# Kernel tuning notes

Measured on AMD Instinct MI355X. Metric: run time of the kernel, lower is better.

Reference implementation:

```python
import math
import jax, jax.numpy as jnp
import numpy as np

B, T, C = 4, 2048, 1024
NH, HD = 16, C // 16
FF = 4096
EPS = 1e-5


def _layernorm(x, g, b):
    mu = jnp.mean(x, axis=-1, keepdims=True)
    var = jnp.mean(jnp.square(x - mu), axis=-1, keepdims=True)
    return (x - mu) * jax.lax.rsqrt(var + EPS) * g + b


def _new_gelu(x):
    c = math.sqrt(2.0 / math.pi)
    return 0.5 * x * (1.0 + jnp.tanh(c * (x + 0.044715 * x * x * x)))


def setup_inputs() -> dict:
    key = jax.random.key(0)
    ks = jax.random.split(key, 5)
    s = lambda fan_in: 1.0 / math.sqrt(fan_in)
    return {
        "x": jax.random.normal(ks[0], (B, T, C), jnp.float32),
        "ln1_g": jnp.ones((C,), jnp.float32),
        "ln1_b": jnp.zeros((C,), jnp.float32),
        "w_qkv": jax.random.normal(ks[1], (C, 3 * C), jnp.float32) * s(C),
        "b_qkv": jnp.zeros((3 * C,), jnp.float32),
        "w_attn_proj": jax.random.normal(ks[2], (C, C), jnp.float32) * s(C),
        "b_attn_proj": jnp.zeros((C,), jnp.float32),
        "ln2_g": jnp.ones((C,), jnp.float32),
        "ln2_b": jnp.zeros((C,), jnp.float32),
        "w_fc": jax.random.normal(ks[3], (C, FF), jnp.float32) * s(C),
        "b_fc": jnp.zeros((FF,), jnp.float32),
        "w_mlp_proj": jax.random.normal(ks[4], (FF, C), jnp.float32) * s(FF),
        "b_mlp_proj": jnp.zeros((C,), jnp.float32),
    }


def reference(x, ln1_g, ln1_b, w_qkv, b_qkv, w_attn_proj, b_attn_proj,
              ln2_g, ln2_b, w_fc, b_fc, w_mlp_proj, b_mlp_proj):
    # --- attention branch ---
    h = _layernorm(x, ln1_g, ln1_b)
    qkv = h @ w_qkv + b_qkv                      # [B,T,3C]
    q, k, v = jnp.split(qkv, 3, axis=-1)
    # [B,T,C] -> [B,NH,T,HD]
    to_heads = lambda t: t.reshape(B, T, NH, HD).transpose(0, 2, 1, 3)
    q, k, v = to_heads(q), to_heads(k), to_heads(v)
    scores = jnp.einsum("bhqd,bhkd->bhqk", q, k) / math.sqrt(HD)  # [B,NH,T,T]
    causal = jnp.tril(jnp.ones((T, T), bool))
    scores = jnp.where(causal, scores, -jnp.inf)
    probs = jax.nn.softmax(scores, axis=-1)
    attn = jnp.einsum("bhqk,bhkd->bhqd", probs, v)  # [B,NH,T,HD]
    attn = attn.transpose(0, 2, 1, 3).reshape(B, T, C)
    x = x + attn @ w_attn_proj + b_attn_proj
    # --- MLP branch ---
    h = _layernorm(x, ln2_g, ln2_b)
    h = _new_gelu(h @ w_fc + b_fc)
    x = x + h @ w_mlp_proj + b_mlp_proj
    return x
```

## Files before the change

### kernel.cpp

```cpp
#include <hip/hip_runtime.h>
#include <hip/hip_bf16.h>

typedef __bf16 bf16x8 __attribute__((ext_vector_type(8)));
typedef __bf16 bf16x4 __attribute__((ext_vector_type(4)));
typedef float f32x4 __attribute__((ext_vector_type(4)));

#define BM 128
#define BN 128
#define BK 32

__device__ __forceinline__ void gload16(const __bf16* g, __bf16* l) {
    __builtin_amdgcn_global_load_lds((const __attribute__((address_space(1))) void*)g,
                                     (__attribute__((address_space(3))) void*)l, 16, 0, 0);
}

__device__ __forceinline__ float gelu_f(float v) {
    float z = 0.7978845608028654f * (v + 0.044715f * v * v * v);
    float e = __expf(2.f * z);
    return 0.5f * v * (2.f - 2.f / (e + 1.f));
}

__global__ __launch_bounds__(256) void diag_kernel(float* out, int n, float v) {
    int i = blockIdx.x * 256 + threadIdx.x;
    if (i < n) out[i] = v;
}

__global__ __launch_bounds__(256) void cvtT_kernel(
    const float* __restrict__ in, __bf16* __restrict__ out, int K, int N)
{
    __shared__ __bf16 tile[32][33];
    int bx = blockIdx.x * 32, by = blockIdx.y * 32;
    int tx = threadIdx.x & 31, ty = threadIdx.x >> 5;
#pragma unroll
    for (int i = 0; i < 32; i += 8)
        tile[ty + i][tx] = (__bf16)in[(size_t)(by + ty + i) * N + bx + tx];
    __syncthreads();
#pragma unroll
    for (int i = 0; i < 32; i += 8)
        out[(size_t)(bx + ty + i) * K + by + tx] = tile[tx][ty + i];
}

__global__ __launch_bounds__(256) void ln_kernel(
    const float* __restrict__ x, const float* __restrict__ g,
    const float* __restrict__ bta, __bf16* __restrict__ out)
{
    const int row = blockIdx.x, t = threadIdx.x;
    const float* xr = x + (size_t)row * 1024;
    float4 xv = ((const float4*)xr)[t];
    float f[4] = {xv.x, xv.y, xv.z, xv.w};
    float s = f[0] + f[1] + f[2] + f[3];
    float ss = f[0]*f[0] + f[1]*f[1] + f[2]*f[2] + f[3]*f[3];
#pragma unroll
    for (int off = 32; off; off >>= 1) {
        s  += __shfl_xor(s, off, 64);
        ss += __shfl_xor(ss, off, 64);
    }
    __shared__ float red[8];
    int lane = t & 63, w = t >> 6;
    if (lane == 0) { red[w] = s; red[4 + w] = ss; }
    __syncthreads();
    s  = red[0] + red[1] + red[2] + red[3];
    ss = red[4] + red[5] + red[6] + red[7];
    float mu = s * (1.f / 1024.f);
    float var = ss * (1.f / 1024.f) - mu * mu;
    float rstd = rsqrtf(fmaxf(var, 0.f) + 1e-5f);
    float4 gv = ((const float4*)g)[t];
    float4 bv = ((const float4*)bta)[t];
    bf16x4 ov;
    ov[0] = (__bf16)((f[0] - mu) * rstd * gv.x + bv.x);
    ov[1] = (__bf16)((f[1] - mu) * rstd * gv.y + bv.y);
    ov[2] = (__bf16)((f[2] - mu) * rstd * gv.z + bv.z);
    ov[3] = (__bf16)((f[3] - mu) * rstd * gv.w + bv.w);
    ((bf16x4*)(out + (size_t)row * 1024))[t] = ov;
}

template <int EPI, bool OUT32>
__global__ __launch_bounds__(256, 4) void gemm_bt_kernel(
    const __bf16* __restrict__ A, const __bf16* __restrict__ BT,
    const float* __restrict__ bias, const float* __restrict__ res,
    void* __restrict__ Cp, int M, int N, int K)
{
    __shared__ __align__(16) __bf16 lA[BM * BK];
    __shared__ __align__(16) __bf16 lB[BN * BK];
    const int t = threadIdx.x;
    const int lane = t & 63;
    const int wave = t >> 6;
    const int wm = wave >> 1, wn = wave & 1;
    const int q4 = lane >> 4, r16 = lane & 15;
    const int bm = blockIdx.y * BM, bn = blockIdx.x * BN;

    const int srow = t & 127;
    const int skc = t >> 7;
    const __bf16* ga0 = A + (size_t)(bm + srow) * K + skc * 8;
    const __bf16* ga1 = A + (size_t)(bm + srow) * K + (skc + 2) * 8;
    const __bf16* gb0 = BT + (size_t)(bn + srow) * K + skc * 8;
    const __bf16* gb1 = BT + (size_t)(bn + srow) * K + (skc + 2) * 8;

    f32x4 acc[4][4];
    f32x4 zero4 = {0.f, 0.f, 0.f, 0.f};
#pragma unroll
    for (int mi = 0; mi < 4; ++mi)
#pragma unroll
        for (int ni = 0; ni < 4; ++ni) acc[mi][ni] = zero4;

    for (int k0 = 0; k0 < K; k0 += BK) {
        __syncthreads();
        gload16(ga0, &lA[t * 8]);
        gload16(ga1, &lA[t * 8 + 2048]);
        gload16(gb0, &lB[t * 8]);
        gload16(gb1, &lB[t * 8 + 2048]);
        ga0 += BK; ga1 += BK; gb0 += BK; gb1 += BK;
        __syncthreads();
        bf16x8 af[4], bfr[4];
#pragma unroll
        for (int i = 0; i < 4; ++i)
            af[i] = *(const bf16x8*)&lA[q4 * 1024 + (wm * 64 + i * 16 + r16) * 8];
#pragma unroll
        for (int i = 0; i < 4; ++i)
            bfr[i] = *(const bf16x8*)&lB[q4 * 1024 + (wn * 64 + i * 16 + r16) * 8];
#pragma unroll
        for (int mi = 0; mi < 4; ++mi)
#pragma unroll
            for (int ni = 0; ni < 4; ++ni)
                acc[mi][ni] = __builtin_amdgcn_mfma_f32_16x16x32_bf16(
                    af[mi], bfr[ni], acc[mi][ni], 0, 0, 0);
    }

#pragma unroll
    for (int mi = 0; mi < 4; ++mi) {
#pragma unroll
        for (int ni = 0; ni < 4; ++ni) {
#pragma unroll
            for (int i = 0; i < 4; ++i) {
                int r = bm + wm * 64 + mi * 16 + q4 * 4 + i;
                int c = bn + wn * 64 + ni * 16 + r16;
                float v = acc[mi][ni][i] + bias[c];
                if (EPI == 1) v += res[(size_t)r * N + c];
                if (EPI == 2) v = gelu_f(v);
                if (OUT32) ((float*)Cp)[(size_t)r * N + c] = v;
                else       ((__bf16*)Cp)[(size_t)r * N + c] = (__bf16)v;
            }
        }
    }
}

template <int EPI, bool OUT32>
__global__ __launch_bounds__(256, 2) void gemm_bt_wide_kernel(
    const __bf16* __restrict__ A, const __bf16* __restrict__ BT,
    const float* __restrict__ bias, const float* __restrict__ res,
    void* __restrict__ Cp, int M, int N, int K)
{
    __shared__ __align__(16) __bf16 lA[128 * BK];
    __shared__ __align__(16) __bf16 lB[256 * BK];
    const int t = threadIdx.x;
    const int lane = t & 63;
    const int wave = t >> 6;
    const int wm = wave >> 1, wn = wave & 1;
    const int q4 = lane >> 4, r16 = lane & 15;
    const int bm = blockIdx.y * 128, bn = blockIdx.x * 256;

    const int srow = t & 127;
    const int skc = t >> 7;
    const __bf16* ga0 = A + (size_t)(bm + srow) * K + skc * 8;
    const __bf16* ga1 = A + (size_t)(bm + srow) * K + (skc + 2) * 8;
    const __bf16* gb  = BT + (size_t)(bn + t) * K;

    f32x4 acc[4][8];
    f32x4 zero4 = {0.f, 0.f, 0.f, 0.f};
#pragma unroll
    for (int mi = 0; mi < 4; ++mi)
#pragma unroll
        for (int ni = 0; ni < 8; ++ni) acc[mi][ni] = zero4;

    for (int k0 = 0; k0 < K; k0 += BK) {
        __syncthreads();
        gload16(ga0, &lA[t * 8]);
        gload16(ga1, &lA[t * 8 + 2048]);
#pragma unroll
        for (int c = 0; c < 4; ++c)
            gload16(gb + c * 8, &lB[c * 2048 + t * 8]);
        ga0 += BK; ga1 += BK; gb += BK;
        __syncthreads();
        bf16x8 af[4], bfr[8];
#pragma unroll
        for (int i = 0; i < 4; ++i)
            af[i] = *(const bf16x8*)&lA[q4 * 1024 + (wm * 64 + i * 16 + r16) * 8];
#pragma unroll
        for (int i = 0; i < 8; ++i)
            bfr[i] = *(const bf16x8*)&lB[q4 * 2048 + (wn * 128 + i * 16 + r16) * 8];
#pragma unroll
        for (int mi = 0; mi < 4; ++mi)
#pragma unroll
            for (int ni = 0; ni < 8; ++ni)
                acc[mi][ni] = __builtin_amdgcn_mfma_f32_16x16x32_bf16(
                    af[mi], bfr[ni], acc[mi][ni], 0, 0, 0);
    }

#pragma unroll
    for (int mi = 0; mi < 4; ++mi) {
#pragma unroll
        for (int ni = 0; ni < 8; ++ni) {
#pragma unroll
            for (int i = 0; i < 4; ++i) {
                int r = bm + wm * 64 + mi * 16 + q4 * 4 + i;
                int c = bn + wn * 128 + ni * 16 + r16;
                float v = acc[mi][ni][i] + bias[c];
                if (EPI == 1) v += res[(size_t)r * N + c];
                if (EPI == 2) v = gelu_f(v);
                if (OUT32) ((float*)Cp)[(size_t)r * N + c] = v;
                else       ((__bf16*)Cp)[(size_t)r * N + c] = (__bf16)v;
            }
        }
    }
}

__global__ __launch_bounds__(256, 4) void attn_kernel(
    const __bf16* __restrict__ qkv, __bf16* __restrict__ attnb)
{
    __shared__ __align__(16) __bf16 lK[8192];
    __shared__ __align__(16) __bf16 lV[8192];
    __shared__ __align__(16) __bf16 lP[4][512];

    const int t = threadIdx.x, lane = t & 63, w = t >> 6;
    const int q4 = lane >> 4, r16 = lane & 15;
    const int b = blockIdx.y >> 4, h = blockIdx.y & 15;
    const int qt = (blockIdx.x + (blockIdx.y >> 4) * 4) & 15;
    const int qb = qt * 128;
    const __bf16* Qb = qkv + (size_t)b * 2048 * 3072 + h * 64;
    const __bf16* Kb = Qb + 1024;
    const __bf16* Vb = Qb + 2048;

    bf16x8 qf[2][2];
#pragma unroll
    for (int p = 0; p < 2; ++p) {
        int qrow = qb + p * 64 + w * 16 + r16;
        qf[p][0] = *(const bf16x8*)(Qb + (size_t)qrow * 3072 + q4 * 8);
        qf[p][1] = *(const bf16x8*)(Qb + (size_t)qrow * 3072 + 32 + q4 * 8);
#pragma unroll
        for (int j = 0; j < 8; ++j) {
            qf[p][0][j] = (__bf16)((float)qf[p][0][j] * 0.125f);
            qf[p][1][j] = (__bf16)((float)qf[p][1][j] * 0.125f);
        }
    }

    f32x4 zero4 = {0.f, 0.f, 0.f, 0.f};
    f32x4 o[2][4];
    float rs[2][4];
#pragma unroll
    for (int p = 0; p < 2; ++p)
#pragma unroll
        for (int i = 0; i < 4; ++i) { o[p][i] = zero4; rs[p][i] = 0.f; }

    const int skey = t & 127;
    const int vkc = t >> 6, svd = t & 63;

    for (int kb = 0; kb < qb + 128; kb += 128) {
        __syncthreads();
#pragma unroll
        for (int c = 0; c < 4; ++c)
            gload16(Kb + (size_t)(kb + skey) * 3072 + (c * 2 + (t >> 7)) * 8,
                    &lK[c * 2048 + t * 8]);
#pragma unroll
        for (int c = 0; c < 4; ++c) {
            int kc = c * 4 + vkc;
            bf16x8 vt;
#pragma unroll
            for (int j = 0; j < 8; ++j)
                vt[j] = Vb[(size_t)(kb + kc * 8 + j) * 3072 + svd];
            *(bf16x8*)&lV[kc * 512 + svd * 8] = vt;
        }
        __syncthreads();

#pragma unroll
        for (int p = 0; p < 2; ++p) {
            const int row0 = qb + p * 64 + w * 16 + q4 * 4;
            const bool interior = (kb + 127) <= (qb + p * 64 + w * 16);

            f32x4 s[8];
#pragma unroll
            for (int kg = 0; kg < 8; ++kg) {
                bf16x8 kfA = *(const bf16x8*)&lK[q4 * 1024 + (kg * 16 + r16) * 8];
                bf16x8 kfB = *(const bf16x8*)&lK[(4 + q4) * 1024 + (kg * 16 + r16) * 8];
                s[kg] = __builtin_amdgcn_mfma_f32_16x16x32_bf16(qf[p][0], kfA, zero4, 0, 0, 0);
                s[kg] = __builtin_amdgcn_mfma_f32_16x16x32_bf16(qf[p][1], kfB, s[kg], 0, 0, 0);
            }

#pragma unroll
            for (int kg = 0; kg < 8; ++kg)
#pragma unroll
                for (int i = 0; i < 4; ++i) {
                    float e = __expf(fminf(s[kg][i], 75.f));
                    if (!interior && (kb + kg * 16 + r16) > (row0 + i)) e = 0.f;
                    s[kg][i] = e;
                    rs[p][i] += e;
                }

#pragma unroll
            for (int c = 0; c < 4; ++c) {
#pragma unroll
                for (int kh = 0; kh < 2; ++kh)
#pragma unroll
                    for (int i = 0; i < 4; ++i)
                        lP[w][(kh * 2 + (r16 >> 3)) * 128 + (q4 * 4 + i) * 8 + (r16 & 7)] =
                            (__bf16)s[c * 2 + kh][i];
                asm volatile("s_waitcnt lgkmcnt(0)" ::: "memory");
                bf16x8 pf = *(const bf16x8*)&lP[w][q4 * 128 + r16 * 8];
#pragma unroll
                for (int ci = 0; ci < 4; ++ci) {
                    bf16x8 vf = *(const bf16x8*)&lV[(c * 4 + q4) * 512 + (ci * 16 + r16) * 8];
                    o[p][ci] = __builtin_amdgcn_mfma_f32_16x16x32_bf16(pf, vf, o[p][ci], 0, 0, 0);
                }
            }
        }
    }

#pragma unroll
    for (int p = 0; p < 2; ++p) {
#pragma unroll
        for (int off = 8; off; off >>= 1)
#pragma unroll
            for (int i = 0; i < 4; ++i) rs[p][i] += __shfl_xor(rs[p][i], off, 64);
#pragma unroll
        for (int ci = 0; ci < 4; ++ci)
#pragma unroll
            for (int i = 0; i < 4; ++i) {
                int trow = qb + p * 64 + w * 16 + q4 * 4 + i;
                float inv_l = (rs[p][i] > 0.f) ? (1.f / rs[p][i]) : 0.f;
                attnb[(size_t)(b * 2048 + trow) * 1024 + h * 64 + ci * 16 + r16] =
                    (__bf16)(o[p][ci][i] * inv_l);
            }
    }
}

extern "C" void kernel_launch(void* const* d_in, const int* in_sizes, int n_in,
                              void* d_out, int out_size, void* d_ws, size_t ws_size,
                              hipStream_t stream)
{
    const float* x      = (const float*)d_in[0];
    const float* ln1_g  = (const float*)d_in[1];
    const float* ln1_b  = (const float*)d_in[2];
    const float* w_qkv  = (const float*)d_in[3];
    const float* b_qkv  = (const float*)d_in[4];
    const float* w_proj = (const float*)d_in[5];
    const float* b_proj = (const float*)d_in[6];
    const float* ln2_g  = (const float*)d_in[7];
    const float* ln2_b  = (const float*)d_in[8];
    const float* w_fc   = (const float*)d_in[9];
    const float* b_fc   = (const float*)d_in[10];
    const float* w_mlp  = (const float*)d_in[11];
    const float* b_mlp  = (const float*)d_in[12];
    float* out = (float*)d_out;

    const size_t MiB = (size_t)1 << 20;
    if (ws_size < 136 * MiB) {
        float v = 1000.f + (float)(ws_size >> 20);
        diag_kernel<<<(out_size + 255) / 256, 256, 0, stream>>>(out, out_size, v);
        return;
    }

    char* ws = (char*)d_ws;
    __bf16* bufA   = (__bf16*)(ws);
    __bf16* bufB   = (__bf16*)(ws + 16 * MiB);
    float*  x1     = (float*) (ws + 80 * MiB);
    __bf16* wqkvT  = (__bf16*)(ws + 112 * MiB);
    __bf16* wprojT = (__bf16*)(ws + 118 * MiB);
    __bf16* wfcT   = (__bf16*)(ws + 120 * MiB);
    __bf16* wmlpT  = (__bf16*)(ws + 128 * MiB);

    cvtT_kernel<<<dim3(96, 32),  256, 0, stream>>>(w_qkv,  wqkvT,  1024, 3072);
    cvtT_kernel<<<dim3(32, 32),  256, 0, stream>>>(w_proj, wprojT, 1024, 1024);
    cvtT_kernel<<<dim3(128, 32), 256, 0, stream>>>(w_fc,   wfcT,   1024, 4096);
    cvtT_kernel<<<dim3(32, 128), 256, 0, stream>>>(w_mlp,  wmlpT,  4096, 1024);

    ln_kernel<<<8192, 256, 0, stream>>>(x, ln1_g, ln1_b, bufA);
    gemm_bt_wide_kernel<0, false><<<dim3(12, 64), 256, 0, stream>>>(
        bufA, wqkvT, b_qkv, nullptr, bufB, 8192, 3072, 1024);
    attn_kernel<<<dim3(16, 64), 256, 0, stream>>>(bufB, bufA);
    gemm_bt_kernel<1, true><<<dim3(8, 64), 256, 0, stream>>>(
        bufA, wprojT, b_proj, x, x1, 8192, 1024, 1024);
    ln_kernel<<<8192, 256, 0, stream>>>(x1, ln2_g, ln2_b, bufA);
    gemm_bt_wide_kernel<2, false><<<dim3(16, 64), 256, 0, stream>>>(
        bufA, wfcT, b_fc, nullptr, bufB, 8192, 4096, 1024);
    gemm_bt_kernel<1, true><<<dim3(8, 64), 256, 0, stream>>>(
        bufB, wmlpT, b_mlp, x1, out, 8192, 1024, 4096);
}
```

Measured before the change: 712.8 us.

## Double-buffer GEMM LDS tiles and split-K the MLP projection with atomics

Both GEMM kernels now double-buffer their LDS tiles. The next K-tile's global-to-LDS loads are issued before the MFMAs on the current tile, which drops one barrier per iteration and overlaps load latency with compute. The final MLP projection (K=4096) is split into two K halves across blockIdx.z and accumulated with float atomicAdd. To make that work, the second LayerNorm pass pre-initializes the output with residual plus bias. This doubles LDS use per block, which may reduce occupancy, and adds atomic traffic and a non-deterministic summation order.

New measurement: 743.0 us. +4.2%, slower.

```diff
diff --git a/kernel.cpp b/kernel.cpp
--- a/kernel.cpp
+++ b/kernel.cpp
@@ -42,7 +42,8 @@
 
 __global__ __launch_bounds__(256) void ln_kernel(
     const float* __restrict__ x, const float* __restrict__ g,
-    const float* __restrict__ bta, __bf16* __restrict__ out)
+    const float* __restrict__ bta, __bf16* __restrict__ out,
+    const float* __restrict__ bias2, float* __restrict__ out2)
 {
     const int row = blockIdx.x, t = threadIdx.x;
     const float* xr = x + (size_t)row * 1024;
@@ -72,29 +73,36 @@
     ov[2] = (__bf16)((f[2] - mu) * rstd * gv.z + bv.z);
     ov[3] = (__bf16)((f[3] - mu) * rstd * gv.w + bv.w);
     ((bf16x4*)(out + (size_t)row * 1024))[t] = ov;
-}
-
-template <int EPI, bool OUT32>
+    if (out2) {
+        float4 b2 = ((const float4*)bias2)[t];
+        float4 o2 = {f[0] + b2.x, f[1] + b2.y, f[2] + b2.z, f[3] + b2.w};
+        ((float4*)(out2 + (size_t)row * 1024))[t] = o2;
+    }
+}
+
+template <int EPI, bool OUT32, int NSPLIT>
 __global__ __launch_bounds__(256, 4) void gemm_bt_kernel(
     const __bf16* __restrict__ A, const __bf16* __restrict__ BT,
     const float* __restrict__ bias, const float* __restrict__ res,
-    void* __restrict__ Cp, int M, int N, int K)
-{
-    __shared__ __align__(16) __bf16 lA[BM * BK];
-    __shared__ __align__(16) __bf16 lB[BN * BK];
+    void* __restrict__ Cp, int M, int N, int K, int lda, int ldb)
+{
+    __shared__ __align__(16) __bf16 lA[2][BM * BK];
+    __shared__ __align__(16) __bf16 lB[2][BN * BK];
     const int t = threadIdx.x;
     const int lane = t & 63;
     const int wave = t >> 6;
     const int wm = wave >> 1, wn = wave & 1;
     const int q4 = lane >> 4, r16 = lane & 15;
     const int bm = blockIdx.y * BM, bn = blockIdx.x * BN;
+    const int Klen = K / NSPLIT;
+    const int koff = (NSPLIT > 1) ? (int)blockIdx.z * Klen : 0;
 
     const int srow = t & 127;
     const int skc = t >> 7;
-    const __bf16* ga0 = A + (size_t)(bm + srow) * K + skc * 8;
-    const __bf16* ga1 = A + (size_t)(bm + srow) * K + (skc + 2) * 8;
-    const __bf16* gb0 = BT + (size_t)(bn + srow) * K + skc * 8;
-    const __bf16* gb1 = BT + (size_t)(bn + srow) * K + (skc + 2) * 8;
+    const __bf16* ga0 = A + (size_t)(bm + srow) * lda + koff + skc * 8;
+    const __bf16* ga1 = ga0 + 16;
+    const __bf16* gb0 = BT + (size_t)(bn + srow) * ldb + koff + skc * 8;
+    const __bf16* gb1 = gb0 + 16;
 
     f32x4 acc[4][4];
     f32x4 zero4 = {0.f, 0.f, 0.f, 0.f};
@@ -103,27 +111,38 @@
 #pragma unroll
         for (int ni = 0; ni < 4; ++ni) acc[mi][ni] = zero4;
 
-    for (int k0 = 0; k0 < K; k0 += BK) {
-        __syncthreads();
-        gload16(ga0, &lA[t * 8]);
-        gload16(ga1, &lA[t * 8 + 2048]);
-        gload16(gb0, &lB[t * 8]);
-        gload16(gb1, &lB[t * 8 + 2048]);
-        ga0 += BK; ga1 += BK; gb0 += BK; gb1 += BK;
-        __syncthreads();
+    gload16(ga0, &lA[0][t * 8]);
+    gload16(ga1, &lA[0][t * 8 + 2048]);
+    gload16(gb0, &lB[0][t * 8]);
+    gload16(gb1, &lB[0][t * 8 + 2048]);
+    ga0 += BK; ga1 += BK; gb0 += BK; gb1 += BK;
+    __syncthreads();
+
+    const int nk = Klen / BK;
+    int cur = 0;
+    for (int it = 0; it < nk; ++it) {
+        if (it + 1 < nk) {
+            gload16(ga0, &lA[cur ^ 1][t * 8]);
+            gload16(ga1, &lA[cur ^ 1][t * 8 + 2048]);
+            gload16(gb0, &lB[cur ^ 1][t * 8]);
+            gload16(gb1, &lB[cur ^ 1][t * 8 + 2048]);
+            ga0 += BK; ga1 += BK; gb0 += BK; gb1 += BK;
+        }
         bf16x8 af[4], bfr[4];
 #pragma unroll
         for (int i = 0; i < 4; ++i)
-            af[i] = *(const bf16x8*)&lA[q4 * 1024 + (wm * 64 + i * 16 + r16) * 8];
+            af[i] = *(const bf16x8*)&lA[cur][q4 * 1024 + (wm * 64 + i * 16 + r16) * 8];
 #pragma unroll
         for (int i = 0; i < 4; ++i)
-            bfr[i] = *(const bf16x8*)&lB[q4 * 1024 + (wn * 64 + i * 16 + r16) * 8];
+            bfr[i] = *(const bf16x8*)&lB[cur][q4 * 1024 + (wn * 64 + i * 16 + r16) * 8];
 #pragma unroll
         for (int mi = 0; mi < 4; ++mi)
 #pragma unroll
             for (int ni = 0; ni < 4; ++ni)
                 acc[mi][ni] = __builtin_amdgcn_mfma_f32_16x16x32_bf16(
                     af[mi], bfr[ni], acc[mi][ni], 0, 0, 0);
+        if (it + 1 < nk) __syncthreads();
+        cur ^= 1;
     }
 
 #pragma unroll
@@ -134,11 +153,15 @@
             for (int i = 0; i < 4; ++i) {
                 int r = bm + wm * 64 + mi * 16 + q4 * 4 + i;
                 int c = bn + wn * 64 + ni * 16 + r16;
-                float v = acc[mi][ni][i] + bias[c];
-                if (EPI == 1) v += res[(size_t)r * N + c];
-                if (EPI == 2) v = gelu_f(v);
-                if (OUT32) ((float*)Cp)[(size_t)r * N + c] = v;
-                else       ((__bf16*)Cp)[(size_t)r * N + c] = (__bf16)v;
+                if (EPI == 3) {
+                    atomicAdd((float*)Cp + (size_t)r * N + c, acc[mi][ni][i]);
+                } else {
+                    float v = acc[mi][ni][i] + bias[c];
+                    if (EPI == 1) v += res[(size_t)r * N + c];
+                    if (EPI == 2) v = gelu_f(v);
+                    if (OUT32) ((float*)Cp)[(size_t)r * N + c] = v;
+                    else       ((__bf16*)Cp)[(size_t)r * N + c] = (__bf16)v;
+                }
             }
         }
     }
@@ -150,8 +173,8 @@
     const float* __restrict__ bias, const float* __restrict__ res,
     void* __restrict__ Cp, int M, int N, int K)
 {
-    __shared__ __align__(16) __bf16 lA[128 * BK];
-    __shared__ __align__(16) __bf16 lB[256 * BK];
+    __shared__ __align__(16) __bf16 lA[2][128 * BK];
+    __shared__ __align__(16) __bf16 lB[2][256 * BK];
     const int t = threadIdx.x;
     const int lane = t & 63;
     const int wave = t >> 6;
@@ -162,7 +185,7 @@
     const int srow = t & 127;
     const int skc = t >> 7;
     const __bf16* ga0 = A + (size_t)(bm + srow) * K + skc * 8;
-    const __bf16* ga1 = A + (size_t)(bm + srow) * K + (skc + 2) * 8;
+    const __bf16* ga1 = ga0 + 16;
     const __bf16* gb  = BT + (size_t)(bn + t) * K;
 
     f32x4 acc[4][8];
@@ -172,28 +195,40 @@
 #pragma unroll
         for (int ni = 0; ni < 8; ++ni) acc[mi][ni] = zero4;
 
-    for (int k0 = 0; k0 < K; k0 += BK) {
-        __syncthreads();
-        gload16(ga0, &lA[t * 8]);
-        gload16(ga1, &lA[t * 8 + 2048]);
-#pragma unroll
-        for (int c = 0; c < 4; ++c)
-            gload16(gb + c * 8, &lB[c * 2048 + t * 8]);
-        ga0 += BK; ga1 += BK; gb += BK;
-        __syncthreads();
+    gload16(ga0, &lA[0][t * 8]);
+    gload16(ga1, &lA[0][t * 8 + 2048]);
+#pragma unroll
+    for (int c = 0; c < 4; ++c)
+        gload16(gb + c * 8, &lB[0][c * 2048 + t * 8]);
+    ga0 += BK; ga1 += BK; gb += BK;
+    __syncthreads();
+
+    const int nk = K / BK;
+    int cur = 0;
+    for (int it = 0; it < nk; ++it) {
+        if (it + 1 < nk) {
+            gload16(ga0, &lA[cur ^ 1][t * 8]);
+            gload16(ga1, &lA[cur ^ 1][t * 8 + 2048]);
+#pragma unroll
+            for (int c = 0; c < 4; ++c)
+                gload16(gb + c * 8, &lB[cur ^ 1][c * 2048 + t * 8]);
+            ga0 += BK; ga1 += BK; gb += BK;
+        }
         bf16x8 af[4], bfr[8];
 #pragma unroll
         for (int i = 0; i < 4; ++i)
-            af[i] = *(const bf16x8*)&lA[q4 * 1024 + (wm * 64 + i * 16 + r16) * 8];
+            af[i] = *(const bf16x8*)&lA[cur][q4 * 1024 + (wm * 64 + i * 16 + r16) * 8];
 #pragma unroll
         for (int i = 0; i < 8; ++i)
-            bfr[i] = *(const bf16x8*)&lB[q4 * 2048 + (wn * 128 + i * 16 + r16) * 8];
+            bfr[i] = *(const bf16x8*)&lB[cur][q4 * 2048 + (wn * 128 + i * 16 + r16) * 8];
 #pragma unroll
         for (int mi = 0; mi < 4; ++mi)
 #pragma unroll
             for (int ni = 0; ni < 8; ++ni)
                 acc[mi][ni] = __builtin_amdgcn_mfma_f32_16x16x32_bf16(
                     af[mi], bfr[ni], acc[mi][ni], 0, 0, 0);
+        if (it + 1 < nk) __syncthreads();
+        cur ^= 1;
     }
 
 #pragma unroll
@@ -372,15 +407,15 @@
     cvtT_kernel<<<dim3(128, 32), 256, 0, stream>>>(w_fc,   wfcT,   1024, 4096);
     cvtT_kernel<<<dim3(32, 128), 256, 0, stream>>>(w_mlp,  wmlpT,  4096, 1024);
 
-    ln_kernel<<<8192, 256, 0, stream>>>(x, ln1_g, ln1_b, bufA);
+    ln_kernel<<<8192, 256, 0, stream>>>(x, ln1_g, ln1_b, bufA, nullptr, nullptr);
     gemm_bt_wide_kernel<0, false><<<dim3(12, 64), 256, 0, stream>>>(
         bufA, wqkvT, b_qkv, nullptr, bufB, 8192, 3072, 1024);
     attn_kernel<<<dim3(16, 64), 256, 0, stream>>>(bufB, bufA);
-    gemm_bt_kernel<1, true><<<dim3(8, 64), 256, 0, stream>>>(
-        bufA, wprojT, b_proj, x, x1, 8192, 1024, 1024);
-    ln_kernel<<<8192, 256, 0, stream>>>(x1, ln2_g, ln2_b, bufA);
+    gemm_bt_kernel<1, true, 1><<<dim3(8, 64), 256, 0, stream>>>(
+        bufA, wprojT, b_proj, x, x1, 8192, 1024, 1024, 1024, 1024);
+    ln_kernel<<<8192, 256, 0, stream>>>(x1, ln2_g, ln2_b, bufA, b_mlp, out);
     gemm_bt_wide_kernel<2, false><<<dim3(16, 64), 256, 0, stream>>>(
         bufA, wfcT, b_fc, nullptr, bufB, 8192, 4096, 1024);
-    gemm_bt_kernel<1, true><<<dim3(8, 64), 256, 0, stream>>>(
-        bufB, wmlpT, b_mlp, x1, out, 8192, 1024, 4096);
-}
+    gemm_bt_kernel<3, true, 2><<<dim3(8, 64, 2), 256, 0, stream>>>(
+        bufB, wmlpT, b_mlp, nullptr, out, 8192, 1024, 4096, 4096, 4096);
+}
```
